# Performance work log

Hardware: AMD Instinct MI355X
Metric: run time of the kernel (lower is better)

The kernel has to match this reference:

```python
import jax, jax.numpy as jnp
import numpy as np

B, T, D = 2, 2048, 1024
H = 16
HD = D // H  # head_dim = 64 (kv_rank == embed_dim)
INT4_MIN, INT4_MAX = -8.0, 7.0


def _int4_quant_dequant(x):
    # per-token amax over last dim (head_dim), as in INT4Quantizer with 4-D input
    amax = jnp.max(jnp.abs(x), axis=-1, keepdims=True)
    amax = jnp.maximum(amax, 1e-5)
    scale = amax / 7.0
    q = jnp.clip(jnp.round(x / scale), INT4_MIN, INT4_MAX)  # stored as int8 in cache
    return q * scale


def setup_inputs() -> dict:
    key = jax.random.key(0)
    ks = jax.random.split(key, 11)
    s = 1.0 / np.sqrt(D)
    return {
        "query": jax.random.normal(ks[0], (B, T, D), jnp.float32),
        "key": jax.random.normal(ks[1], (B, T, D), jnp.float32),
        "value": jax.random.normal(ks[2], (B, T, D), jnp.float32),
        "Wq": jax.random.normal(ks[3], (D, D), jnp.float32) * s,
        "bq": jnp.zeros((D,), jnp.float32),
        "Wk": jax.random.normal(ks[4], (D, D), jnp.float32) * s,
        "bk": jnp.zeros((D,), jnp.float32),
        "Wv": jax.random.normal(ks[5], (D, D), jnp.float32) * s,
        "bv": jnp.zeros((D,), jnp.float32),
        "Wo": jax.random.normal(ks[6], (D, D), jnp.float32) * s,
        "bo": jnp.zeros((D,), jnp.float32),
    }


def reference(query, key, value, Wq, bq, Wk, bk, Wv, bv, Wo, bo):
    # projections (nn.Linear: x @ W.T + b)
    q = query @ Wq.T + bq
    k = key @ Wk.T + bk
    v = value @ Wv.T + bv
    # (B, T, D) -> (B, H, T, HD)
    q = q.reshape(B, T, H, HD).transpose(0, 2, 1, 3)
    k = k.reshape(B, T, H, HD).transpose(0, 2, 1, 3)
    v = v.reshape(B, T, H, HD).transpose(0, 2, 1, 3)
    # INT4 quantized KV cache update (use_cache=True): quantize -> scatter into
    # fresh cache -> dequantize the just-written block == quant/dequant of k, v
    k = _int4_quant_dequant(k)
    v = _int4_quant_dequant(v)
    # attention
    scale = HD ** (-0.5)
    attn = jnp.einsum("bhqd,bhkd->bhqk", q, k) * scale
    attn = jax.nn.softmax(attn.astype(jnp.float32), axis=-1).astype(query.dtype)
    out = jnp.einsum("bhqk,bhkd->bhqd", attn, v)
    out = out.transpose(0, 2, 1, 3).reshape(B, T, D)
    out = out @ Wo.T + bo
    return out
```

## Files before the change

### kernel.cpp

```cpp
#include <hip/hip_runtime.h>

typedef unsigned short u16;
typedef unsigned int u32;
typedef float f32x4 __attribute__((ext_vector_type(4)));
typedef float f32x16 __attribute__((ext_vector_type(16)));
typedef short s16x8 __attribute__((ext_vector_type(8)));
typedef u16 u16x8 __attribute__((ext_vector_type(8)));
typedef u16 u16x4 __attribute__((ext_vector_type(4)));
typedef u32 u32x4 __attribute__((ext_vector_type(4)));
typedef _Float16 h16x8 __attribute__((ext_vector_type(8)));
typedef _Float16 h16x2 __attribute__((ext_vector_type(2)));

#define B_ 2
#define T_ 2048
#define H_ 16
#define D_ 1024
#define HD_ 64
#define NTOK (B_*T_)

#define QSCALE 0.18033688011112042f

__device__ __forceinline__ u16 f2b(float f){
  u32 u = __float_as_uint(f);
  return (u16)((u + 0x7fffu + ((u>>16)&1u)) >> 16);
}
__device__ __forceinline__ float b2f(u16 h){ return __uint_as_float(((u32)h)<<16); }

__device__ __forceinline__ void gload_lds16(const u16* g, u16* s){
  __builtin_amdgcn_global_load_lds((const __attribute__((address_space(1))) void*)g,
                                   (__attribute__((address_space(3))) void*)s, 16, 0, 0);
}

template<int ROWS, int WAVES>
__device__ __forceinline__ void stage_tile(const u16* __restrict__ g, size_t ldg,
                                           u16* s, int tid){
  const int w = tid>>6, l = tid&63;
  const int rw = ROWS/WAVES;
  #pragma unroll
  for (int i=0;i<ROWS/(WAVES*8);i++){
    int r0 = w*rw + i*8;
    int r  = r0 + (l>>3);
    int u  = (l&7) ^ (r&7);
    gload_lds16(g + (size_t)r*ldg + (size_t)u*8, s + r0*64);
  }
}

__device__ __forceinline__ u16x8 rfragT(const u16* s, int r, int ks, int hi){
  int phys = (ks*2 + hi) ^ (r&7);
  return *(const u16x8*)(s + r*64 + phys*8);
}

__device__ __forceinline__ void stage_tile32(const u16* __restrict__ g, size_t ldg,
                                             u16* s, int tid){
  const int w = tid>>6, l = tid&63;
  int r0 = w*16;
  int r  = r0 + (l>>2);
  int v  = (l&3) ^ ((r>>1)&3);
  gload_lds16(g + (size_t)r*ldg + (size_t)v*8, s + r0*32);
}
__device__ __forceinline__ u16x8 read_frag32(const u16* s, int r, int l){
  int phys = (l>>4) ^ ((r>>1)&3);
  return *(const u16x8*)(s + r*32 + phys*8);
}

__device__ __forceinline__ f32x4 mfma16_bf16(u16x8 a, u16x8 b, f32x4 c){
  return __builtin_amdgcn_mfma_f32_16x16x32_bf16(
      __builtin_bit_cast(s16x8,a), __builtin_bit_cast(s16x8,b), c, 0,0,0);
}
__device__ __forceinline__ f32x16 mfma32_f16(u16x8 a, u16x8 b, f32x16 c){
  return __builtin_amdgcn_mfma_f32_32x32x16_f16(
      __builtin_bit_cast(h16x8,a), __builtin_bit_cast(h16x8,b), c, 0,0,0);
}

__device__ __forceinline__ float ex2(float x){
#if __has_builtin(__builtin_amdgcn_exp2f)
  return __builtin_amdgcn_exp2f(x);
#else
  return exp2f(x);
#endif
}
__device__ __forceinline__ u32 pk2(float a, float b){
  u16 x = __builtin_bit_cast(u16, (_Float16)a);
  u16 y = __builtin_bit_cast(u16, (_Float16)b);
  return (u32)x | ((u32)y<<16);
}
__device__ __forceinline__ u32 pkrtz(float a, float b){
#if __has_builtin(__builtin_amdgcn_cvt_pkrtz)
  auto r = __builtin_amdgcn_cvt_pkrtz(a, b);
  return __builtin_bit_cast(u32, r);
#else
  return pk2(a, b);
#endif
}

__device__ __forceinline__ void split_bf4(const float* in, u16* hi, u16* lo, int i){
  f32x4 v = ((const f32x4*)in)[i];
  u16x4 h, lw;
  #pragma unroll
  for (int j=0;j<4;j++){
    u16 hb = f2b(v[j]);
    h[j] = hb;
    lw[j] = f2b(v[j] - b2f(hb));
  }
  ((u16x4*)hi)[i] = h;
  ((u16x4*)lo)[i] = lw;
}
__device__ __forceinline__ void split_h4(const float* in, u16* out, int i){
  f32x4 v = ((const f32x4*)in)[i];
  u16x4 o;
  #pragma unroll
  for (int j=0;j<4;j++){
    _Float16 t = (_Float16)v[j];
    o[j] = __builtin_bit_cast(u16, t);
  }
  ((u16x4*)out)[i] = o;
}

__global__ void split_all_kernel(const float* __restrict__ q, const float* __restrict__ k,
                                 const float* __restrict__ v,
                                 const float* __restrict__ wq, const float* __restrict__ wk,
                                 const float* __restrict__ wv, const float* __restrict__ wo,
                                 u16* __restrict__ qh, u16* __restrict__ khi, u16* __restrict__ klo,
                                 u16* __restrict__ vhi, u16* __restrict__ vlo,
                                 u16* __restrict__ wqh, u16* __restrict__ wkh, u16* __restrict__ wkl,
                                 u16* __restrict__ wvh, u16* __restrict__ wvl, u16* __restrict__ woh){
  int i = blockIdx.x*256 + threadIdx.x;
  int which = blockIdx.y;
  if (which < 3){
    if (which==0)      split_h4 (q, qh, i);
    else if (which==1) split_bf4(k, khi, klo, i);
    else               split_bf4(v, vhi, vlo, i);
  } else {
    if (i >= D_*D_/4) return;
    if (which==3)      split_h4 (wq, wqh, i);
    else if (which==4) split_bf4(wk, wkh, wkl, i);
    else if (which==5) split_bf4(wv, wvh, wvl, i);
    else               split_h4 (wo, woh, i);
  }
}

template<int F16OUT>
__global__ __launch_bounds__(256)
void gemm1(const u16* __restrict__ Ah, const u16* __restrict__ Wh,
           const float* __restrict__ bias, void* __restrict__ Cout, float oscale)
{
  __shared__ u16 sA[2][128*64];
  __shared__ u16 sW[2][128*64];
  const int tid = threadIdx.x, l = tid&63, c = l&31, hi = l>>5, w = tid>>6;
  const int wm = w>>1, wn = w&1;
  const int bm = blockIdx.x, bn = blockIdx.y;
  const u16* A0 = Ah + (size_t)bm*128*D_;
  const u16* W0 = Wh + (size_t)bn*128*D_;
  f32x16 acc[2][2] = {};

  stage_tile<128,4>(A0, D_, sA[0], tid);
  stage_tile<128,4>(W0, D_, sW[0], tid);
  __syncthreads();
  for (int t=0; t<D_/64; ++t){
    const int cur = t&1;
    if (t+1 < D_/64){
      stage_tile<128,4>(A0 + (t+1)*64, D_, sA[cur^1], tid);
      stage_tile<128,4>(W0 + (t+1)*64, D_, sW[cur^1], tid);
    }
    #pragma unroll
    for (int kc=0;kc<4;kc++){
      u16x8 af[2], wf[2];
      af[0] = rfragT(sA[cur], wm*64 +      c, kc, hi);
      af[1] = rfragT(sA[cur], wm*64 + 32 + c, kc, hi);
      wf[0] = rfragT(sW[cur], wn*64 +      c, kc, hi);
      wf[1] = rfragT(sW[cur], wn*64 + 32 + c, kc, hi);
      #pragma unroll
      for (int mb=0;mb<2;mb++)
        #pragma unroll
        for (int nb=0;nb<2;nb++)
          acc[mb][nb] = mfma32_f16(af[mb], wf[nb], acc[mb][nb]);
    }
    __syncthreads();
  }

  #pragma unroll
  for (int nb=0;nb<2;nb++){
    int col = bn*128 + wn*64 + nb*32 + c;
    float bv = bias[col];
    #pragma unroll
    for (int mb=0;mb<2;mb++){
      #pragma unroll
      for (int r=0;r<16;r++){
        int row = bm*128 + wm*64 + mb*32 + (r&3) + 8*(r>>2) + 4*hi;
        float v = (acc[mb][nb][r] + bv) * oscale;
        if constexpr (F16OUT){
          ((_Float16*)Cout)[(size_t)row*D_ + col] = (_Float16)v;
        } else {
          ((float*)Cout)[(size_t)row*D_ + col] = v;
        }
      }
    }
  }
}

__global__ __launch_bounds__(512)
void gemm3_quant_kv(const u16* __restrict__ kAh, const u16* __restrict__ kAl,
                    const u16* __restrict__ kWh, const u16* __restrict__ kWl,
                    const float* __restrict__ kbias, u16* __restrict__ kOut,
                    const u16* __restrict__ vAh, const u16* __restrict__ vAl,
                    const u16* __restrict__ vWh, const u16* __restrict__ vWl,
                    const float* __restrict__ vbias, u16* __restrict__ vOut)
{
  extern __shared__ u16 sm[];
  const int tid = threadIdx.x, l = tid&63, w = tid>>6, l15 = l&15, g = l>>4;
  const int wm = w>>1, wn = w&1;
  const int bm = blockIdx.x, bn = blockIdx.y;
  const bool isV = blockIdx.z != 0;
  const u16* Ah = isV ? vAh : kAh;
  const u16* Al = isV ? vAl : kAl;
  const u16* Wh = isV ? vWh : kWh;
  const u16* Wl = isV ? vWl : kWl;
  const float* bias = isV ? vbias : kbias;
  u16* Out = isV ? vOut : kOut;

  const u16* A0 = Ah + (size_t)bm*128*D_;
  const u16* A1 = Al + (size_t)bm*128*D_;
  const u16* W0 = Wh + (size_t)bn*128*D_;
  const u16* W1 = Wl + (size_t)bn*128*D_;
  constexpr int TS = 128*32;
  f32x4 acc[2][4] = {};

  auto stage = [&](int buf, int t){
    u16* base = sm + buf*4*TS;
    stage_tile32(A0 + t*32, D_, base       , tid);
    stage_tile32(A1 + t*32, D_, base +   TS, tid);
    stage_tile32(W0 + t*32, D_, base + 2*TS, tid);
    stage_tile32(W1 + t*32, D_, base + 3*TS, tid);
  };
  stage(0,0);
  __syncthreads();
  for (int t=0; t<D_/32; ++t){
    const int cur = t&1;
    if (t+1 < D_/32) stage(cur^1, t+1);
    const u16* base = sm + cur*4*TS;
    u16x8 ahh[2], ahl[2], whh[4], whl[4];
    #pragma unroll
    for (int fm=0;fm<2;fm++){
      ahh[fm] = read_frag32(base     , wm*32+fm*16+l15, l);
      ahl[fm] = read_frag32(base+  TS, wm*32+fm*16+l15, l);
    }
    #pragma unroll
    for (int fn=0;fn<4;fn++){
      whh[fn] = read_frag32(base+2*TS, wn*64+fn*16+l15, l);
      whl[fn] = read_frag32(base+3*TS, wn*64+fn*16+l15, l);
    }
    #pragma unroll
    for (int fm=0;fm<2;fm++)
      #pragma unroll
      for (int fn=0;fn<4;fn++){
        acc[fm][fn] = mfma16_bf16(ahh[fm], whh[fn], acc[fm][fn]);
        acc[fm][fn] = mfma16_bf16(ahh[fm], whl[fn], acc[fm][fn]);
        acc[fm][fn] = mfma16_bf16(ahl[fm], whh[fn], acc[fm][fn]);
      }
    __syncthreads();
  }

  #pragma unroll
  for (int fn=0;fn<4;fn++){
    float bv = bias[bn*128 + wn*64 + fn*16 + l15];
    #pragma unroll
    for (int fm=0;fm<2;fm++)
      #pragma unroll
      for (int j=0;j<4;j++) acc[fm][fn][j] += bv;
  }

  u16 (*sdq)[136] = (u16(*)[136])sm;
  #pragma unroll
  for (int fm=0;fm<2;fm++)
    #pragma unroll
    for (int j=0;j<4;j++){
      float a = 0.f;
      #pragma unroll
      for (int fn=0;fn<4;fn++) a = fmaxf(a, fabsf(acc[fm][fn][j]));
      a = fmaxf(a, __shfl_xor(a,1)); a = fmaxf(a, __shfl_xor(a,2));
      a = fmaxf(a, __shfl_xor(a,4)); a = fmaxf(a, __shfl_xor(a,8));
      a = fmaxf(a, 1e-5f);
      float scale = a / 7.0f;
      int g2 = ((g&1)<<1) | (g>>1);
      int rowK = wm*32 + fm*16 + g*4  + j;
      int rowV = wm*32 + fm*16 + g2*4 + j;
      #pragma unroll
      for (int fn=0;fn<4;fn++){
        float q = rintf(acc[fm][fn][j] / scale);
        q = fminf(fmaxf(q, -8.f), 7.f);
        _Float16 dq = (_Float16)(q * scale);
        int col = wn*64 + fn*16 + l15;
        if (!isV) sdq[rowK][col] = __builtin_bit_cast(u16, dq);
        else      sdq[col][rowV] = __builtin_bit_cast(u16, dq);
      }
    }
  __syncthreads();

  if (!isV){
    int r = tid>>2, seg = tid&3;
    u16* dst = Out + (size_t)(bm*128 + r)*D_ + bn*128 + seg*32;
    #pragma unroll
    for (int i=0;i<4;i++)
      *(u16x8*)(dst + i*8) = *(const u16x8*)&sdq[r][seg*32 + i*8];
  } else {
    int cc = tid>>2, seg = tid&3;
    int hh = 2*bn + (cc>>6), dd = cc&63, b = bm>>4;
    u16* dst = Out + ((size_t)((b*H_+hh)*HD_ + dd))*T_ + (bm&15)*128 + seg*32;
    #pragma unroll
    for (int i=0;i<4;i++)
      *(u16x8*)(dst + i*8) = *(const u16x8*)&sdq[cc][seg*32 + i*8];
  }
}

__global__ __launch_bounds__(256, 4)
void attn_kernel(const _Float16* __restrict__ Qp, const u16* __restrict__ Kdq,
                 const u16* __restrict__ Vt, float* __restrict__ po,
                 float* __restrict__ pl)
{
  __shared__ u16 sK[2][64*64];
  __shared__ u16 sV[2][64*64];
  const int tid = threadIdx.x, l = tid&63, c = l&31, hi = l>>5, w = tid>>6;
  const int dsp = blockIdx.x;
  const int xcd = dsp & 7, slot = dsp >> 3;
  const int bh = xcd*4 + (slot>>5);
  const int rem = slot & 31;
  const int qb = rem >> 1, sp = rem & 1;
  const int b = bh>>4, h = bh&15;

  u16x8 qf[4];
  {
    const u16* qrow = (const u16*)Qp + (size_t)(b*T_ + qb*128 + w*32 + c)*D_ + h*HD_;
    #pragma unroll
    for (int ks=0;ks<4;ks++)
      qf[ks] = *(const u16x8*)(qrow + ks*16 + hi*8);
  }

  f32x16 o0 = {}, o1 = {};
  float lsp = 0.f;

  const u16* Kb = Kdq + (size_t)(b*T_ + sp*1024)*D_ + h*HD_;
  const u16* Vb = Vt  + (size_t)(bh*HD_)*T_ + sp*1024;

  stage_tile<64,4>(Kb, D_, sK[0], tid);
  stage_tile<64,4>(Vb, T_, sV[0], tid);
  __syncthreads();

  for (int kt=0; kt<16; kt++){
    const int cur = kt&1;
    if (kt+1 < 16){
      stage_tile<64,4>(Kb + (size_t)((kt+1)*64)*D_, D_, sK[cur^1], tid);
      stage_tile<64,4>(Vb + (kt+1)*64,              T_, sV[cur^1], tid);
    }
    const u16* sKc = sK[cur];
    const u16* sVc = sV[cur];

    u16x8 vf0[4], vf1[4];
    #pragma unroll
    for (int ch=0; ch<4; ch++){
      vf0[ch] = rfragT(sVc,      c, ch, hi);
      vf1[ch] = rfragT(sVc, 32 + c, ch, hi);
    }

    #pragma unroll
    for (int kb=0;kb<2;kb++){
      f32x16 s = {};
      #pragma unroll
      for (int ks=0;ks<4;ks++){
        u16x8 kf = rfragT(sKc, kb*32 + c, ks, hi);
        s = mfma32_f16(kf, qf[ks], s);
      }
      float p[16];
      #pragma unroll
      for (int r=0;r<16;r++) p[r] = ex2(s[r]);
      {
        float t0 = (p[0]+p[1]) + (p[2]+p[3]);
        float t1 = (p[4]+p[5]) + (p[6]+p[7]);
        float t2 = (p[8]+p[9]) + (p[10]+p[11]);
        float t3 = (p[12]+p[13]) + (p[14]+p[15]);
        lsp += (t0+t1) + (t2+t3);
      }
      u32x4 pw0 = { pkrtz(p[0],p[1]),  pkrtz(p[2],p[3]),
                    pkrtz(p[4],p[5]),  pkrtz(p[6],p[7]) };
      u32x4 pw1 = { pkrtz(p[8],p[9]),  pkrtz(p[10],p[11]),
                    pkrtz(p[12],p[13]),pkrtz(p[14],p[15]) };
      u16x8 pa0 = __builtin_bit_cast(u16x8, pw0);
      u16x8 pa1 = __builtin_bit_cast(u16x8, pw1);
      o0 = mfma32_f16(pa0, vf0[kb*2+0], o0);
      o0 = mfma32_f16(pa1, vf0[kb*2+1], o0);
      o1 = mfma32_f16(pa0, vf1[kb*2+0], o1);
      o1 = mfma32_f16(pa1, vf1[kb*2+1], o1);
    }
    __syncthreads();
  }

  float lt = lsp + __shfl_xor(lsp, 32);
  if (hi == 0) pl[(size_t)(sp*32 + bh)*T_ + qb*128 + w*32 + c] = lt;

  float* pob = po + ((size_t)(sp*32 + bh)*T_ + qb*128 + w*32)*HD_;
  #pragma unroll
  for (int r=0;r<16;r++){
    int crow = (r&3) + 8*(r>>2) + 4*hi;
    pob[crow*HD_ + c]      = o0[r];
    pob[crow*HD_ + 32 + c] = o1[r];
  }
}

__global__ __launch_bounds__(256)
void combine_kernel(const float* __restrict__ po, const float* __restrict__ pl,
                    u16* __restrict__ Ao)
{
  int i = blockIdx.x*256 + threadIdx.x;
  int d4 = (i & 15) * 4;
  int t  = (i >> 4) & (T_-1);
  int bh = i >> 15;
  size_t r0 = ((size_t)bh*T_ + t);
  f32x4 a = *(const f32x4*)(po + r0*HD_ + d4);
  f32x4 b = *(const f32x4*)(po + (r0 + (size_t)32*T_)*HD_ + d4);
  float lt = pl[r0] + pl[r0 + (size_t)32*T_];
  float rl = 1.0f / lt;
  u16x4 o;
  #pragma unroll
  for (int j=0;j<4;j++)
    o[j] = __builtin_bit_cast(u16, (_Float16)((a[j]+b[j])*rl));
  int bb = bh>>4, hh = bh&15;
  *(u16x4*)(Ao + ((size_t)(bb*T_ + t))*D_ + hh*HD_ + d4) = o;
}

extern "C" void kernel_launch(void* const* d_in, const int* in_sizes, int n_in,
                              void* d_out, int out_size, void* d_ws, size_t ws_size,
                              hipStream_t stream)
{
  (void)in_sizes; (void)n_in; (void)out_size; (void)ws_size;
  const float* query = (const float*)d_in[0];
  const float* key   = (const float*)d_in[1];
  const float* value = (const float*)d_in[2];
  const float* Wq = (const float*)d_in[3];
  const float* bq = (const float*)d_in[4];
  const float* Wk = (const float*)d_in[5];
  const float* bk = (const float*)d_in[6];
  const float* Wv = (const float*)d_in[7];
  const float* bv = (const float*)d_in[8];
  const float* Wo = (const float*)d_in[9];
  const float* bo = (const float*)d_in[10];
  float* out = (float*)d_out;

  char* p = (char*)d_ws;
  auto take = [&](size_t n){ char* r = p; p += (n + 255) & ~(size_t)255; return r; };
  const size_t big = (size_t)NTOK*D_*2;
  const size_t wsz = (size_t)D_*D_*2;

  u16* q_h  = (u16*)take(big);
  u16* khi  = (u16*)take(big);  u16* klo = (u16*)take(big);
  u16* vhi  = (u16*)take(big);  u16* vlo = (u16*)take(big);
  u16* wq_h = (u16*)take(wsz);
  u16* wkh  = (u16*)take(wsz);  u16* wkl = (u16*)take(wsz);
  u16* wvh  = (u16*)take(wsz);  u16* wvl = (u16*)take(wsz);
  u16* wo_h = (u16*)take(wsz);
  u16*  Qp  = (u16*)take(big);
  u16*  Kdq = (u16*)take(big);
  u16*  Vtp = (u16*)take(big);
  u16*  Ao  = (u16*)take(big);

  float* po = (float*)khi;
  float* pl = (float*)wq_h;

  split_all_kernel<<<dim3(NTOK*D_/4/256, 7), 256, 0, stream>>>(
      query, key, value, Wq, Wk, Wv, Wo,
      q_h, khi, klo, vhi, vlo,
      wq_h, wkh, wkl, wvh, wvl, wo_h);

  gemm1<1><<<dim3(32,8), 256, 0, stream>>>(q_h, wq_h, bq, Qp, QSCALE);

  gemm3_quant_kv<<<dim3(32,8,2), 512, 64*1024, stream>>>(
      khi, klo, wkh, wkl, bk, Kdq,
      vhi, vlo, wvh, wvl, bv, Vtp);

  attn_kernel<<<1024, 256, 0, stream>>>((const _Float16*)Qp, Kdq, Vtp, po, pl);
  combine_kernel<<<4096, 256, 0, stream>>>(po, pl, Ao);

  gemm1<0><<<dim3(32,8), 256, 0, stream>>>(Ao, wo_h, bo, out, 1.0f);
}
```

Before: 177.3 us.

## Rework K/V split-bf16 GEMM to 32x32 MFMA tiles with 4 waves and K=64 stages

The fused K/V projection-plus-INT4-quantize kernel moves from 8 waves using 16x16x32 bf16 MFMAs with 32-wide K stages to 4 waves using 32x32x16 bf16 MFMAs with 64-wide K stages, reusing the swizzled stage_tile/rfragT helpers. Each wave now computes a 64x64 output tile, which raises register-level reuse and halves the number of barriers per K. The per-row amax reduction and the transposed V store into LDS are rewritten for the 32x32 accumulator layout. Shared memory becomes a static 128KB buffer. Fewer waves per block may reduce latency hiding, and the larger LDS footprint limits occupancy.

Result: slower. 195.4 us (+10.2%).

```diff
diff --git a/kernel.cpp b/kernel.cpp
--- a/kernel.cpp
+++ b/kernel.cpp
@@ -50,26 +50,13 @@
   return *(const u16x8*)(s + r*64 + phys*8);
 }
 
-__device__ __forceinline__ void stage_tile32(const u16* __restrict__ g, size_t ldg,
-                                             u16* s, int tid){
-  const int w = tid>>6, l = tid&63;
-  int r0 = w*16;
-  int r  = r0 + (l>>2);
-  int v  = (l&3) ^ ((r>>1)&3);
-  gload_lds16(g + (size_t)r*ldg + (size_t)v*8, s + r0*32);
-}
-__device__ __forceinline__ u16x8 read_frag32(const u16* s, int r, int l){
-  int phys = (l>>4) ^ ((r>>1)&3);
-  return *(const u16x8*)(s + r*32 + phys*8);
-}
-
-__device__ __forceinline__ f32x4 mfma16_bf16(u16x8 a, u16x8 b, f32x4 c){
-  return __builtin_amdgcn_mfma_f32_16x16x32_bf16(
-      __builtin_bit_cast(s16x8,a), __builtin_bit_cast(s16x8,b), c, 0,0,0);
-}
 __device__ __forceinline__ f32x16 mfma32_f16(u16x8 a, u16x8 b, f32x16 c){
   return __builtin_amdgcn_mfma_f32_32x32x16_f16(
       __builtin_bit_cast(h16x8,a), __builtin_bit_cast(h16x8,b), c, 0,0,0);
+}
+__device__ __forceinline__ f32x16 mfma32_bf16(u16x8 a, u16x8 b, f32x16 c){
+  return __builtin_amdgcn_mfma_f32_32x32x16_bf16(
+      __builtin_bit_cast(s16x8,a), __builtin_bit_cast(s16x8,b), c, 0,0,0);
 }
 
 __device__ __forceinline__ float ex2(float x){
@@ -198,7 +185,7 @@
   }
 }
 
-__global__ __launch_bounds__(512)
+__global__ __launch_bounds__(256)
 void gemm3_quant_kv(const u16* __restrict__ kAh, const u16* __restrict__ kAl,
                     const u16* __restrict__ kWh, const u16* __restrict__ kWl,
                     const float* __restrict__ kbias, u16* __restrict__ kOut,
@@ -206,8 +193,8 @@
                     const u16* __restrict__ vWh, const u16* __restrict__ vWl,
                     const float* __restrict__ vbias, u16* __restrict__ vOut)
 {
-  extern __shared__ u16 sm[];
-  const int tid = threadIdx.x, l = tid&63, w = tid>>6, l15 = l&15, g = l>>4;
+  __shared__ u16 sm[2*4*128*64];
+  const int tid = threadIdx.x, l = tid&63, c = l&31, hi = l>>5, w = tid>>6;
   const int wm = w>>1, wn = w&1;
   const int bm = blockIdx.x, bn = blockIdx.y;
   const bool isV = blockIdx.z != 0;
@@ -216,99 +203,107 @@
   const u16* Wh = isV ? vWh : kWh;
   const u16* Wl = isV ? vWl : kWl;
   const float* bias = isV ? vbias : kbias;
-  u16* Out = isV ? vOut : kOut;
-
+
+  constexpr int TS = 128*64;
   const u16* A0 = Ah + (size_t)bm*128*D_;
   const u16* A1 = Al + (size_t)bm*128*D_;
   const u16* W0 = Wh + (size_t)bn*128*D_;
   const u16* W1 = Wl + (size_t)bn*128*D_;
-  constexpr int TS = 128*32;
-  f32x4 acc[2][4] = {};
+
+  f32x16 acc[2][2] = {};
 
   auto stage = [&](int buf, int t){
     u16* base = sm + buf*4*TS;
-    stage_tile32(A0 + t*32, D_, base       , tid);
-    stage_tile32(A1 + t*32, D_, base +   TS, tid);
-    stage_tile32(W0 + t*32, D_, base + 2*TS, tid);
-    stage_tile32(W1 + t*32, D_, base + 3*TS, tid);
+    stage_tile<128,4>(A0 + t*64, D_, base       , tid);
+    stage_tile<128,4>(A1 + t*64, D_, base +   TS, tid);
+    stage_tile<128,4>(W0 + t*64, D_, base + 2*TS, tid);
+    stage_tile<128,4>(W1 + t*64, D_, base + 3*TS, tid);
   };
   stage(0,0);
   __syncthreads();
-  for (int t=0; t<D_/32; ++t){
+  for (int t=0; t<D_/64; ++t){
     const int cur = t&1;
-    if (t+1 < D_/32) stage(cur^1, t+1);
+    if (t+1 < D_/64) stage(cur^1, t+1);
     const u16* base = sm + cur*4*TS;
-    u16x8 ahh[2], ahl[2], whh[4], whl[4];
-    #pragma unroll
-    for (int fm=0;fm<2;fm++){
-      ahh[fm] = read_frag32(base     , wm*32+fm*16+l15, l);
-      ahl[fm] = read_frag32(base+  TS, wm*32+fm*16+l15, l);
-    }
-    #pragma unroll
-    for (int fn=0;fn<4;fn++){
-      whh[fn] = read_frag32(base+2*TS, wn*64+fn*16+l15, l);
-      whl[fn] = read_frag32(base+3*TS, wn*64+fn*16+l15, l);
-    }
-    #pragma unroll
-    for (int fm=0;fm<2;fm++)
-      #pragma unroll
-      for (int fn=0;fn<4;fn++){
-        acc[fm][fn] = mfma16_bf16(ahh[fm], whh[fn], acc[fm][fn]);
-        acc[fm][fn] = mfma16_bf16(ahh[fm], whl[fn], acc[fm][fn]);
-        acc[fm][fn] = mfma16_bf16(ahl[fm], whh[fn], acc[fm][fn]);
-      }
+    #pragma unroll
+    for (int kc=0;kc<4;kc++){
+      u16x8 ah[2], al[2], wh[2], wl[2];
+      #pragma unroll
+      for (int mb=0;mb<2;mb++){
+        int r = wm*64 + mb*32 + c;
+        ah[mb] = rfragT(base     , r, kc, hi);
+        al[mb] = rfragT(base+  TS, r, kc, hi);
+      }
+      #pragma unroll
+      for (int nb=0;nb<2;nb++){
+        int r = wn*64 + nb*32 + c;
+        wh[nb] = rfragT(base+2*TS, r, kc, hi);
+        wl[nb] = rfragT(base+3*TS, r, kc, hi);
+      }
+      #pragma unroll
+      for (int mb=0;mb<2;mb++)
+        #pragma unroll
+        for (int nb=0;nb<2;nb++){
+          acc[mb][nb] = mfma32_bf16(ah[mb], wh[nb], acc[mb][nb]);
+          acc[mb][nb] = mfma32_bf16(ah[mb], wl[nb], acc[mb][nb]);
+          acc[mb][nb] = mfma32_bf16(al[mb], wh[nb], acc[mb][nb]);
+        }
+    }
     __syncthreads();
   }
 
-  #pragma unroll
-  for (int fn=0;fn<4;fn++){
-    float bv = bias[bn*128 + wn*64 + fn*16 + l15];
-    #pragma unroll
-    for (int fm=0;fm<2;fm++)
-      #pragma unroll
-      for (int j=0;j<4;j++) acc[fm][fn][j] += bv;
-  }
+  float bv[2];
+  #pragma unroll
+  for (int nb=0;nb<2;nb++) bv[nb] = bias[bn*128 + wn*64 + nb*32 + c];
+  #pragma unroll
+  for (int mb=0;mb<2;mb++)
+    #pragma unroll
+    for (int nb=0;nb<2;nb++)
+      #pragma unroll
+      for (int r=0;r<16;r++) acc[mb][nb][r] += bv[nb];
 
   u16 (*sdq)[136] = (u16(*)[136])sm;
   #pragma unroll
-  for (int fm=0;fm<2;fm++)
-    #pragma unroll
-    for (int j=0;j<4;j++){
-      float a = 0.f;
-      #pragma unroll
-      for (int fn=0;fn<4;fn++) a = fmaxf(a, fabsf(acc[fm][fn][j]));
-      a = fmaxf(a, __shfl_xor(a,1)); a = fmaxf(a, __shfl_xor(a,2));
-      a = fmaxf(a, __shfl_xor(a,4)); a = fmaxf(a, __shfl_xor(a,8));
+  for (int mb=0;mb<2;mb++)
+    #pragma unroll
+    for (int r=0;r<16;r++){
+      float a = fmaxf(fabsf(acc[mb][0][r]), fabsf(acc[mb][1][r]));
+      a = fmaxf(a, __shfl_xor(a,1));  a = fmaxf(a, __shfl_xor(a,2));
+      a = fmaxf(a, __shfl_xor(a,4));  a = fmaxf(a, __shfl_xor(a,8));
+      a = fmaxf(a, __shfl_xor(a,16));
       a = fmaxf(a, 1e-5f);
       float scale = a / 7.0f;
-      int g2 = ((g&1)<<1) | (g>>1);
-      int rowK = wm*32 + fm*16 + g*4  + j;
-      int rowV = wm*32 + fm*16 + g2*4 + j;
-      #pragma unroll
-      for (int fn=0;fn<4;fn++){
-        float q = rintf(acc[fm][fn][j] / scale);
+      int crow = (r&3) + 8*(r>>2) + 4*hi;
+      #pragma unroll
+      for (int nb=0;nb<2;nb++){
+        float q = rintf(acc[mb][nb][r] / scale);
         q = fminf(fmaxf(q, -8.f), 7.f);
-        _Float16 dq = (_Float16)(q * scale);
-        int col = wn*64 + fn*16 + l15;
-        if (!isV) sdq[rowK][col] = __builtin_bit_cast(u16, dq);
-        else      sdq[col][rowV] = __builtin_bit_cast(u16, dq);
+        u16 dq = __builtin_bit_cast(u16, (_Float16)(q * scale));
+        if (!isV){
+          int row_l = wm*64 + mb*32 + crow;
+          sdq[row_l][wn*64 + nb*32 + c] = dq;
+        } else {
+          int slot = (crow & 16) | (crow & 3) | (((crow>>3)&1)<<2) | (hi<<3);
+          int row_l = wm*64 + mb*32 + slot;
+          sdq[wn*64 + nb*32 + c][row_l] = dq;
+        }
       }
     }
   __syncthreads();
 
   if (!isV){
-    int r = tid>>2, seg = tid&3;
-    u16* dst = Out + (size_t)(bm*128 + r)*D_ + bn*128 + seg*32;
-    #pragma unroll
-    for (int i=0;i<4;i++)
-      *(u16x8*)(dst + i*8) = *(const u16x8*)&sdq[r][seg*32 + i*8];
+    int rr = tid>>1, seg = tid&1;
+    u16* dst = kOut + (size_t)(bm*128 + rr)*D_ + bn*128 + seg*64;
+    #pragma unroll
+    for (int i=0;i<8;i++)
+      *(u16x8*)(dst + i*8) = *(const u16x8*)&sdq[rr][seg*64 + i*8];
   } else {
-    int cc = tid>>2, seg = tid&3;
+    int cc = tid>>1, seg = tid&1;
     int hh = 2*bn + (cc>>6), dd = cc&63, b = bm>>4;
-    u16* dst = Out + ((size_t)((b*H_+hh)*HD_ + dd))*T_ + (bm&15)*128 + seg*32;
-    #pragma unroll
-    for (int i=0;i<4;i++)
-      *(u16x8*)(dst + i*8) = *(const u16x8*)&sdq[cc][seg*32 + i*8];
+    u16* dst = vOut + ((size_t)((b*H_+hh)*HD_ + dd))*T_ + (bm&15)*128 + seg*64;
+    #pragma unroll
+    for (int i=0;i<8;i++)
+      *(u16x8*)(dst + i*8) = *(const u16x8*)&sdq[cc][seg*64 + i*8];
   }
 }
 
@@ -471,7 +466,7 @@
 
   gemm1<1><<<dim3(32,8), 256, 0, stream>>>(q_h, wq_h, bq, Qp, QSCALE);
 
-  gemm3_quant_kv<<<dim3(32,8,2), 512, 64*1024, stream>>>(
+  gemm3_quant_kv<<<dim3(32,8,2), 256, 0, stream>>>(
       khi, klo, wkh, wkl, bk, Kdq,
       vhi, vlo, wvh, wvl, bv, Vtp);
 
```
